# Performance work log

Hardware: AMD Instinct MI355X
Metric: run time of the kernel (lower is better)

## Reference

```python
import jax, jax.numpy as jnp
import numpy as np

B, N, M = 4, 2048, 2048
DIM, DIM_KEYS, DIM_OUT = 512, 512, 512
HEADS, DIM_HEAD = 8, 64
INNER = HEADS * DIM_HEAD


def setup_inputs() -> dict:
    key = jax.random.key(0)
    ks = jax.random.split(key, 8)
    x = jax.random.normal(ks[0], (B, N, DIM), dtype=jnp.float32)
    context = jax.random.normal(ks[1], (B, M, DIM_KEYS), dtype=jnp.float32)
    Wq = jax.random.normal(ks[2], (DIM, INNER), dtype=jnp.float32) / np.sqrt(DIM)
    Wkv = jax.random.normal(ks[3], (DIM_KEYS, 2 * INNER), dtype=jnp.float32) / np.sqrt(DIM_KEYS)
    null_k = jax.random.normal(ks[4], (DIM_HEAD,), dtype=jnp.float32)
    null_v = jax.random.normal(ks[5], (DIM_HEAD,), dtype=jnp.float32)
    Wout = jax.random.normal(ks[6], (INNER, DIM_OUT), dtype=jnp.float32) / np.sqrt(INNER)
    bout = jnp.zeros((DIM_OUT,), dtype=jnp.float32)
    return {"x": x, "context": context, "Wq": Wq, "Wkv": Wkv,
            "null_k": null_k, "null_v": null_v, "Wout": Wout, "bout": bout}


def reference(x, context, Wq, Wkv, null_k, null_v, Wout, bout):
    b = x.shape[0]
    scale = DIM_HEAD ** (-0.5)
    q = x @ Wq                      # [b, n, inner]
    kv = context @ Wkv              # [b, m, 2*inner]
    k, v = jnp.split(kv, 2, axis=-1)
    # [b, h, n, d]
    q = q.reshape(b, -1, HEADS, DIM_HEAD).transpose(0, 2, 1, 3)
    k = k.reshape(b, -1, HEADS, DIM_HEAD).transpose(0, 2, 1, 3)
    v = v.reshape(b, -1, HEADS, DIM_HEAD).transpose(0, 2, 1, 3)
    # prepend null key/value token: [b, h, 1, d]
    nk = jnp.broadcast_to(null_k, (b, HEADS, 1, DIM_HEAD))
    nv = jnp.broadcast_to(null_v, (b, HEADS, 1, DIM_HEAD))
    k = jnp.concatenate((nk, k), axis=-2)  # [b, h, m+1, d]
    v = jnp.concatenate((nv, v), axis=-2)
    q = jnp.tanh(q)
    k = jnp.tanh(k)
    sim = jnp.einsum('bhid,bhjd->bhij', q, k) * scale  # [b, h, n, m+1]
    attn = jax.nn.softmax(sim, axis=-1)
    out = jnp.einsum('bhij,bhjd->bhid', attn, v)       # [b, h, n, d]
    out = out.transpose(0, 2, 1, 3).reshape(b, -1, INNER)  # [b, n, inner]
    return out @ Wout + bout
```

## Files before the change

kernel.cpp:

```cpp
#include <hip/hip_runtime.h>
#include <hip/hip_bf16.h>
#include <stdint.h>

#define B_    4
#define N_    2048
#define M_    2048
#define DIMX  512
#define INNER 512
#define H_    8
#define DH    64
#define MK    2049
#define MKP   2112

#define QSCALE  0.18033688011f
#define SM_BIAS -11.5415605f

using u16 = unsigned short;
using u32 = unsigned int;

typedef __attribute__((ext_vector_type(8))) short short8;
typedef __attribute__((ext_vector_type(4))) float f32x4;

#if defined(__has_builtin)
# if __has_builtin(__builtin_amdgcn_exp2f)
#  define EXP2(x) __builtin_amdgcn_exp2f(x)
# endif
#endif
#ifndef EXP2
# define EXP2(x) exp2f(x)
#endif

__device__ __forceinline__ u16 bfc(float f){
  __hip_bfloat16 h = __float2bfloat16(f);
  return *reinterpret_cast<u16*>(&h);
}
__device__ __forceinline__ u32 bfpk(float lo, float hi){
  return (u32)bfc(lo) | ((u32)bfc(hi) << 16);
}
__device__ __forceinline__ u32 bfpk_tr(float lo, float hi){
  union { float f; u32 u; } a, b; a.f = lo; b.f = hi;
  return (a.u >> 16) | (b.u & 0xffff0000u);
}

__global__ __launch_bounds__(256) void prep(
    const float* __restrict__ x, const float* __restrict__ ctx,
    const float* __restrict__ Wq, const float* __restrict__ Wkv,
    const float* __restrict__ Wout,
    u16* __restrict__ xb, u16* __restrict__ cb,
    u16* __restrict__ Wqt, u16* __restrict__ Wkvt, u16* __restrict__ Woutt)
{
  const int bid = blockIdx.x;
  if (bid < 4096){
    const float* in = (bid < 2048) ? x : ctx;
    u16* out        = (bid < 2048) ? xb : cb;
    const int i = (bid & 2047) * 256 + threadIdx.x;
    float4 a = ((const float4*)in)[i*2];
    float4 b = ((const float4*)in)[i*2+1];
    uint4 t;
    t.x = bfpk(a.x, a.y); t.y = bfpk(a.z, a.w);
    t.z = bfpk(b.x, b.y); t.w = bfpk(b.z, b.w);
    ((uint4*)out)[i] = t;
    return;
  }
  const int tt = bid - 4096;
  const int z  = tt >> 7;
  const int rem = tt & 127;
  const int cx = rem & 15, ry = rem >> 4;
  const float* in = (z == 0) ? Wq : (z == 1) ? Wkv : Wout;
  u16* out        = (z == 0) ? Wqt : (z == 1) ? Wkvt : Woutt;
  const int C     = (z == 1) ? 1024 : 512;
  const int R     = 512;
  if (cx * 64 >= C) return;

  __shared__ float tl[64][65];
  const int t = threadIdx.x;
  const int c0 = cx * 64, r0 = ry * 64;
  const int col = t & 63, rb = t >> 6;
  #pragma unroll
  for (int j = 0; j < 16; ++j){
    const int row = rb + j*4;
    tl[row][col] = in[(size_t)(r0 + row) * C + c0 + col];
  }
  __syncthreads();
  #pragma unroll
  for (int j = 0; j < 16; ++j){
    const int orow = rb + j*4;
    out[(size_t)(c0 + orow) * R + r0 + col] = bfc(tl[col][orow]);
  }
}

#define PROJ_COMPUTE(bi)                                                      \
  {                                                                           \
    short8 af[4], bf[4];                                                      \
    _Pragma("unroll")                                                         \
    for (int m = 0; m < 4; ++m){                                              \
      const int row = wr + m*16 + c;                                          \
      af[m] = *(const short8*)((char*)At[bi] + row*64 + ((g ^ ((row>>1)&3)) << 4)); \
    }                                                                         \
    _Pragma("unroll")                                                         \
    for (int n = 0; n < 4; ++n){                                              \
      const int row = wc + n*16 + c;                                          \
      bf[n] = *(const short8*)((char*)Bl[bi] + row*64 + ((g ^ ((row>>1)&3)) << 4)); \
    }                                                                         \
    __builtin_amdgcn_s_setprio(1);                                            \
    _Pragma("unroll")                                                         \
    for (int m = 0; m < 4; ++m)                                               \
      _Pragma("unroll")                                                       \
      for (int n = 0; n < 4; ++n)                                             \
        acc[m][n] = __builtin_amdgcn_mfma_f32_16x16x32_bf16(af[m], bf[n], acc[m][n], 0, 0, 0); \
    __builtin_amdgcn_s_setprio(0);                                            \
  }

__global__ __launch_bounds__(256, 3) void fused_proj(
    const u16* __restrict__ xb, const u16* __restrict__ cb,
    const u16* __restrict__ Wqt, const u16* __restrict__ Wkvt,
    u16* __restrict__ qb, u16* __restrict__ kb, u16* __restrict__ vb)
{
  __shared__ __align__(16) short At[2][128*32];
  __shared__ __align__(16) short Bl[2][128*32];

  const int flat = blockIdx.x;
  const int tile = (flat & 7) * 96 + (flat >> 3);
  const bool isq = tile < 256;
  const int lt   = isq ? tile : tile - 256;
  const int gx   = isq ? 4 : 8;
  const int row0 = (lt / gx) * 128, col0 = (lt % gx) * 128;
  const u16* A  = isq ? xb : cb;
  const u16* Bt = isq ? Wqt : Wkvt;

  const int tid = threadIdx.x;
  const int w = tid >> 6, lane = tid & 63;
  const int c = lane & 15, g = lane >> 4;
  const int wr = (w >> 1) * 64, wc = (w & 1) * 64;

  f32x4 acc[4][4] = {};

  const int srow = tid >> 1, sj = (tid & 1) * 2;
  const int swz0 = ((sj  ) ^ ((srow >> 1) & 3)) << 4;
  const int swz1 = ((sj+1) ^ ((srow >> 1) & 3)) << 4;

  const u16* asrc = A  + (size_t)(row0 + srow) * DIMX + sj*8;
  const u16* bsrc = Bt + (size_t)(col0 + srow) * DIMX + sj*8;

  uint4 aA0, aA1, bA0, bA1;
  uint4 aB0, aB1, bB0, bB1;

  aA0 = ((const uint4*)asrc)[0];        aA1 = ((const uint4*)asrc)[1];
  bA0 = ((const uint4*)bsrc)[0];        bA1 = ((const uint4*)bsrc)[1];
  aB0 = ((const uint4*)(asrc + 32))[0]; aB1 = ((const uint4*)(asrc + 32))[1];
  bB0 = ((const uint4*)(bsrc + 32))[0]; bB1 = ((const uint4*)(bsrc + 32))[1];
  *(uint4*)((char*)At[0] + srow*64 + swz0) = aA0;
  *(uint4*)((char*)At[0] + srow*64 + swz1) = aA1;
  *(uint4*)((char*)Bl[0] + srow*64 + swz0) = bA0;
  *(uint4*)((char*)Bl[0] + srow*64 + swz1) = bA1;

  for (int kk = 0; kk < 16; kk += 2){
    __syncthreads();
    if (kk + 2 < 16){
      const u16* an = asrc + (kk+2)*32;
      const u16* bn = bsrc + (kk+2)*32;
      aA0 = ((const uint4*)an)[0]; aA1 = ((const uint4*)an)[1];
      bA0 = ((const uint4*)bn)[0]; bA1 = ((const uint4*)bn)[1];
    }
    PROJ_COMPUTE(0);
    *(uint4*)((char*)At[1] + srow*64 + swz0) = aB0;
    *(uint4*)((char*)At[1] + srow*64 + swz1) = aB1;
    *(uint4*)((char*)Bl[1] + srow*64 + swz0) = bB0;
    *(uint4*)((char*)Bl[1] + srow*64 + swz1) = bB1;

    __syncthreads();
    if (kk + 3 < 16){
      const u16* an = asrc + (kk+3)*32;
      const u16* bn = bsrc + (kk+3)*32;
      aB0 = ((const uint4*)an)[0]; aB1 = ((const uint4*)an)[1];
      bB0 = ((const uint4*)bn)[0]; bB1 = ((const uint4*)bn)[1];
    }
    PROJ_COMPUTE(1);
    if (kk + 2 < 16){
      *(uint4*)((char*)At[0] + srow*64 + swz0) = aA0;
      *(uint4*)((char*)At[0] + srow*64 + swz1) = aA1;
      *(uint4*)((char*)Bl[0] + srow*64 + swz0) = bA0;
      *(uint4*)((char*)Bl[0] + srow*64 + swz1) = bA1;
    }
  }

  #pragma unroll
  for (int m = 0; m < 4; ++m){
    #pragma unroll
    for (int n = 0; n < 4; ++n){
      #pragma unroll
      for (int rr = 0; rr < 4; ++rr){
        const int R = row0 + wr + m*16 + g*4 + rr;
        const int col = col0 + wc + n*16 + c;
        const float v = acc[m][n][rr];
        if (isq){
          qb[(size_t)R * INNER + col] = bfc(tanhf(v) * QSCALE);
        } else {
          const int bidx = R >> 11, mm = R & 2047;
          if (col < INNER){
            const int h = col >> 6, d = col & 63;
            kb[((size_t)(bidx*H_ + h) * MKP + (mm + 1)) * DH + d] = bfc(tanhf(v));
          } else {
            const int cc = col - INNER;
            const int h = cc >> 6, d = cc & 63;
            vb[((size_t)(bidx*H_ + h) * MKP + (mm + 1)) * DH + d] = bfc(v);
          }
        }
      }
    }
  }
}

__global__ __launch_bounds__(256, 3) void mgemm_out(
    const u16* __restrict__ A, const u16* __restrict__ Bt,
    float* __restrict__ Cf, const float* __restrict__ bias)
{
  __shared__ __align__(16) short At[2][128*32];
  __shared__ __align__(16) short Bl[2][64*32];

  const int flat = blockIdx.x;
  const int tile = (flat & 7) * 64 + (flat >> 3);
  const int row0 = (tile >> 3) * 128, col0 = (tile & 7) * 64;

  const int tid = threadIdx.x;
  const int w = tid >> 6, lane = tid & 63;
  const int c = lane & 15, g = lane >> 4;
  const int wr = (w >> 1) * 64, wc = (w & 1) * 32;

  f32x4 acc[4][2] = {};

  const int srow = tid >> 1, sj = (tid & 1) * 2;
  const int swz0 = ((sj  ) ^ ((srow >> 1) & 3)) << 4;
  const int swz1 = ((sj+1) ^ ((srow >> 1) & 3)) << 4;
  const int brow = tid >> 2, bch = tid & 3;
  const int bswz = (bch ^ ((brow >> 1) & 3)) << 4;

  const u16* asrc = A  + (size_t)(row0 + srow) * INNER + sj*8;
  const u16* bsrc = Bt + (size_t)(col0 + brow) * INNER + bch*8;

  uint4 aA0, aA1, bA0;
  uint4 aB0, aB1, bB0;

  aA0 = ((const uint4*)asrc)[0];        aA1 = ((const uint4*)asrc)[1];
  bA0 = *(const uint4*)bsrc;
  aB0 = ((const uint4*)(asrc + 32))[0]; aB1 = ((const uint4*)(asrc + 32))[1];
  bB0 = *(const uint4*)(bsrc + 32);
  *(uint4*)((char*)At[0] + srow*64 + swz0) = aA0;
  *(uint4*)((char*)At[0] + srow*64 + swz1) = aA1;
  *(uint4*)((char*)Bl[0] + brow*64 + bswz) = bA0;

  for (int kk = 0; kk < 16; kk += 2){
    __syncthreads();
    if (kk + 2 < 16){
      const u16* an = asrc + (kk+2)*32;
      aA0 = ((const uint4*)an)[0]; aA1 = ((const uint4*)an)[1];
      bA0 = *(const uint4*)(bsrc + (kk+2)*32);
    }
    {
      short8 af[4], bf[2];
      #pragma unroll
      for (int m = 0; m < 4; ++m){
        const int row = wr + m*16 + c;
        af[m] = *(const short8*)((char*)At[0] + row*64 + ((g ^ ((row>>1)&3)) << 4));
      }
      #pragma unroll
      for (int n = 0; n < 2; ++n){
        const int row = wc + n*16 + c;
        bf[n] = *(const short8*)((char*)Bl[0] + row*64 + ((g ^ ((row>>1)&3)) << 4));
      }
      __builtin_amdgcn_s_setprio(1);
      #pragma unroll
      for (int m = 0; m < 4; ++m)
        #pragma unroll
        for (int n = 0; n < 2; ++n)
          acc[m][n] = __builtin_amdgcn_mfma_f32_16x16x32_bf16(af[m], bf[n], acc[m][n], 0, 0, 0);
      __builtin_amdgcn_s_setprio(0);
    }
    *(uint4*)((char*)At[1] + srow*64 + swz0) = aB0;
    *(uint4*)((char*)At[1] + srow*64 + swz1) = aB1;
    *(uint4*)((char*)Bl[1] + brow*64 + bswz) = bB0;

    __syncthreads();
    if (kk + 3 < 16){
      const u16* an = asrc + (kk+3)*32;
      aB0 = ((const uint4*)an)[0]; aB1 = ((const uint4*)an)[1];
      bB0 = *(const uint4*)(bsrc + (kk+3)*32);
    }
    {
      short8 af[4], bf[2];
      #pragma unroll
      for (int m = 0; m < 4; ++m){
        const int row = wr + m*16 + c;
        af[m] = *(const short8*)((char*)At[1] + row*64 + ((g ^ ((row>>1)&3)) << 4));
      }
      #pragma unroll
      for (int n = 0; n < 2; ++n){
        const int row = wc + n*16 + c;
        bf[n] = *(const short8*)((char*)Bl[1] + row*64 + ((g ^ ((row>>1)&3)) << 4));
      }
      __builtin_amdgcn_s_setprio(1);
      #pragma unroll
      for (int m = 0; m < 4; ++m)
        #pragma unroll
        for (int n = 0; n < 2; ++n)
          acc[m][n] = __builtin_amdgcn_mfma_f32_16x16x32_bf16(af[m], bf[n], acc[m][n], 0, 0, 0);
      __builtin_amdgcn_s_setprio(0);
    }
    if (kk + 2 < 16){
      *(uint4*)((char*)At[0] + srow*64 + swz0) = aA0;
      *(uint4*)((char*)At[0] + srow*64 + swz1) = aA1;
      *(uint4*)((char*)Bl[0] + brow*64 + bswz) = bA0;
    }
  }

  #pragma unroll
  for (int m = 0; m < 4; ++m){
    #pragma unroll
    for (int n = 0; n < 2; ++n){
      #pragma unroll
      for (int rr = 0; rr < 4; ++rr){
        const int R = row0 + wr + m*16 + g*4 + rr;
        const int col = col0 + wc + n*16 + c;
        Cf[(size_t)R * 512 + col] = acc[m][n][rr] + bias[col];
      }
    }
  }
}

__global__ __launch_bounds__(256) void vtrans(
    const u16* __restrict__ vb, u16* __restrict__ vt,
    const float* __restrict__ nk, const float* __restrict__ nv,
    u16* __restrict__ kb)
{
  __shared__ short tl[64][72];
  const int t = threadIdx.x;
  const int mt = blockIdx.x, bh = blockIdx.y;
  {
    const int mr = t >> 2, chb = (t & 3) * 2;
    const u16* src = vb + ((size_t)bh * MKP + mt*64 + mr) * DH + chb*8;
    uint4 a = ((const uint4*)src)[0];
    uint4 b = ((const uint4*)src)[1];
    *(uint4*)((char*)tl + mr*144 + chb*16)     = a;
    *(uint4*)((char*)tl + mr*144 + (chb+1)*16) = b;
  }
  __syncthreads();
  {
    const int d = t >> 2, chb = (t & 3) * 2;
    #pragma unroll
    for (int j = 0; j < 2; ++j){
      const int mbase = (chb + j) * 8;
      u16 s[8];
      #pragma unroll
      for (int e = 0; e < 8; ++e) s[e] = (u16)tl[mbase + e][d];
      if (mt == 0 && mbase == 0) s[0] = bfc(nv[d]);
      uint4 o;
      o.x = (u32)s[0] | ((u32)s[1] << 16);
      o.y = (u32)s[2] | ((u32)s[3] << 16);
      o.z = (u32)s[4] | ((u32)s[5] << 16);
      o.w = (u32)s[6] | ((u32)s[7] << 16);
      *(uint4*)(vt + ((size_t)bh * DH + d) * MKP + mt*64 + mbase) = o;
    }
    if (mt == 0 && (t & 3) == 0)
      kb[(size_t)bh * MKP * DH + d] = bfc(tanhf(nk[d]));
  }
}

__global__ __launch_bounds__(256) void attn_mfma(
    const u16* __restrict__ qb, const u16* __restrict__ kb,
    const u16* __restrict__ vt, u16* __restrict__ aob)
{
  __shared__ __align__(16) short Kl[2][64*64];
  __shared__ __align__(16) short Vl[2][64*64];
  __shared__ __align__(16) short Pl[4][32*64];

  const int tid  = threadIdx.x;
  const int w    = tid >> 6;
  const int lane = tid & 63;
  const int c    = lane & 15;
  const int g    = lane >> 4;
  const int bh   = blockIdx.y, b = bh >> 3, h = bh & 7;
  const int qbase = blockIdx.x * 128 + w * 32;
  const int xr   = (c & 7) << 4;

  short8 qf[2][2];
  #pragma unroll
  for (int u = 0; u < 2; ++u){
    const u16* qrow = qb + ((size_t)(b*N_) + qbase + u*16 + c) * INNER + h * DH;
    qf[u][0] = *(const short8*)(qrow + g*8);
    qf[u][1] = *(const short8*)(qrow + 32 + g*8);
  }

  f32x4 o[2][4] = {};
  f32x4 lacc[2] = {};
  const short8 ones = {0x3F80,0x3F80,0x3F80,0x3F80,0x3F80,0x3F80,0x3F80,0x3F80};

  const u16* kbase = kb + (size_t)bh * MKP * DH;
  const u16* vbase = vt + (size_t)bh * DH * MKP;
  const int srow = tid >> 2, sch = (tid & 3) * 2;
  const int swz0 = ((sch  ) ^ (srow & 7)) << 4;
  const int swz1 = ((sch+1) ^ (srow & 7)) << 4;

  uint4 rk0, rk1, rv0, rv1;
  {
    const u16* ksrc = kbase + (size_t)srow * DH + sch*8;
    rk0 = ((const uint4*)ksrc)[0]; rk1 = ((const uint4*)ksrc)[1];
    const u16* vsrc = vbase + (size_t)srow * MKP + sch*8;
    rv0 = ((const uint4*)vsrc)[0]; rv1 = ((const uint4*)vsrc)[1];
  }
  *(uint4*)((char*)Kl[0] + srow*128 + swz0) = rk0;
  *(uint4*)((char*)Kl[0] + srow*128 + swz1) = rk1;
  *(uint4*)((char*)Vl[0] + srow*128 + swz0) = rv0;
  *(uint4*)((char*)Vl[0] + srow*128 + swz1) = rv1;

  int cur = 0;
  for (int kt = 0; kt < 33; ++kt){
    __syncthreads();
    if (kt < 32){
      const u16* ksrc = kbase + (size_t)((kt+1)*64 + srow) * DH + sch*8;
      rk0 = ((const uint4*)ksrc)[0]; rk1 = ((const uint4*)ksrc)[1];
      const u16* vsrc = vbase + (size_t)srow * MKP + (kt+1)*64 + sch*8;
      rv0 = ((const uint4*)vsrc)[0]; rv1 = ((const uint4*)vsrc)[1];
    }

    const char* Kc = (const char*)Kl[cur];
    const char* Vc = (const char*)Vl[cur];
    char*       Pw = (char*)Pl + w*4096;

    f32x4 sv[2][4];
    __builtin_amdgcn_s_setprio(1);
    #pragma unroll
    for (int s = 0; s < 4; ++s){
      const int row = s*16 + c;
      short8 kf0 = *(const short8*)(Kc + row*128 + ((     g*16) ^ xr));
      short8 kf1 = *(const short8*)(Kc + row*128 + ((64 + g*16) ^ xr));
      f32x4 a0 = {SM_BIAS, SM_BIAS, SM_BIAS, SM_BIAS};
      f32x4 a1 = {SM_BIAS, SM_BIAS, SM_BIAS, SM_BIAS};
      a0 = __builtin_amdgcn_mfma_f32_16x16x32_bf16(kf0, qf[0][0], a0, 0, 0, 0);
      a1 = __builtin_amdgcn_mfma_f32_16x16x32_bf16(kf0, qf[1][0], a1, 0, 0, 0);
      a0 = __builtin_amdgcn_mfma_f32_16x16x32_bf16(kf1, qf[0][1], a0, 0, 0, 0);
      a1 = __builtin_amdgcn_mfma_f32_16x16x32_bf16(kf1, qf[1][1], a1, 0, 0, 0);
      sv[0][s] = a0; sv[1][s] = a1;
    }
    __builtin_amdgcn_s_setprio(0);

    if (kt == 32){
      #pragma unroll
      for (int u = 0; u < 2; ++u)
        #pragma unroll
        for (int s = 0; s < 4; ++s)
          #pragma unroll
          for (int r = 0; r < 4; ++r)
            if (s | r) sv[u][s][r] = -1e30f;
      if (g){ sv[0][0][0] = -1e30f; sv[1][0][0] = -1e30f; }
    }

    #pragma unroll
    for (int u = 0; u < 2; ++u){
      #pragma unroll
      for (int s = 0; s < 4; ++s){
        const float p0 = EXP2(sv[u][s][0]);
        const float p1 = EXP2(sv[u][s][1]);
        const float p2 = EXP2(sv[u][s][2]);
        const float p3 = EXP2(sv[u][s][3]);
        uint2 pk;
        pk.x = bfpk_tr(p0, p1);
        pk.y = bfpk_tr(p2, p3);
        *(uint2*)(Pw + (u*16 + c)*128
                  + ((((2*s + (g>>1)) ^ (c&7)) << 4) | ((g&1)*8))) = pk;
      }
    }

    __builtin_amdgcn_s_setprio(1);
    #pragma unroll
    for (int hh = 0; hh < 2; ++hh){
      short8 pf0 = *(const short8*)(Pw + (     c)*128 + (((hh*4 + g) ^ (c&7)) << 4));
      short8 pf1 = *(const short8*)(Pw + (16 + c)*128 + (((hh*4 + g) ^ (c&7)) << 4));
      lacc[0] = __builtin_amdgcn_mfma_f32_16x16x32_bf16(pf0, ones, lacc[0], 0, 0, 0);
      lacc[1] = __builtin_amdgcn_mfma_f32_16x16x32_bf16(pf1, ones, lacc[1], 0, 0, 0);
      #pragma unroll
      for (int D = 0; D < 4; ++D){
        short8 vf = *(const short8*)(Vc + (D*16 + c)*128 + ((hh*64 + g*16) ^ xr));
        o[0][D] = __builtin_amdgcn_mfma_f32_16x16x32_bf16(pf0, vf, o[0][D], 0, 0, 0);
        o[1][D] = __builtin_amdgcn_mfma_f32_16x16x32_bf16(pf1, vf, o[1][D], 0, 0, 0);
      }
    }
    __builtin_amdgcn_s_setprio(0);

    if (kt < 32){
      char* Kn = (char*)Kl[cur ^ 1];
      char* Vn = (char*)Vl[cur ^ 1];
      *(uint4*)(Kn + srow*128 + swz0) = rk0;
      *(uint4*)(Kn + srow*128 + swz1) = rk1;
      *(uint4*)(Vn + srow*128 + swz0) = rv0;
      *(uint4*)(Vn + srow*128 + swz1) = rv1;
      cur ^= 1;
    }
  }

  #pragma unroll
  for (int u = 0; u < 2; ++u){
    #pragma unroll
    for (int r = 0; r < 4; ++r){
      const float ir = 1.f / lacc[u][r];
      const size_t nrow = (size_t)(b*N_) + qbase + u*16 + g*4 + r;
      #pragma unroll
      for (int D = 0; D < 4; ++D)
        aob[nrow * INNER + h*DH + D*16 + c] = bfc(o[u][D][r] * ir);
    }
  }
}

extern "C" void kernel_launch(void* const* d_in, const int* in_sizes, int n_in,
                              void* d_out, int out_size, void* d_ws, size_t ws_size,
                              hipStream_t stream)
{
  const float* x    = (const float*)d_in[0];
  const float* ctx  = (const float*)d_in[1];
  const float* Wq   = (const float*)d_in[2];
  const float* Wkv  = (const float*)d_in[3];
  const float* nk   = (const float*)d_in[4];
  const float* nv   = (const float*)d_in[5];
  const float* Wout = (const float*)d_in[6];
  const float* bout = (const float*)d_in[7];
  float* out = (float*)d_out;

  char* ws = (char*)d_ws;
  u16* xb    = (u16*)(ws);
  u16* cb    = (u16*)(ws +  8388608);
  u16* qb    = (u16*)(ws + 16777216);
  u16* kbB   = (u16*)(ws + 25165824);
  u16* vbB   = (u16*)(ws + 33816576);
  u16* vtb   = (u16*)(ws + 42467328);
  u16* Wqt   = (u16*)(ws + 51118080);
  u16* Wkvt  = (u16*)(ws + 51642368);
  u16* Woutt = (u16*)(ws + 52690944);
  u16* aoB   = vbB;

  prep<<<4480, 256, 0, stream>>>(x, ctx, Wq, Wkv, Wout, xb, cb, Wqt, Wkvt, Woutt);

  fused_proj<<<768, 256, 0, stream>>>(xb, cb, Wqt, Wkvt, qb, kbB, vbB);
  vtrans<<<dim3(33, 32), 256, 0, stream>>>(vbB, vtb, nk, nv, kbB);
  attn_mfma<<<dim3(16, 32), 256, 0, stream>>>(qb, kbB, vtb, aoB);
  mgemm_out<<<512, 256, 0, stream>>>(aoB, Woutt, out, bout);
}
```

Baseline: 108.9 us.

## Write V transposed directly from projection epilogue and drop vtrans kernel

The projection epilogue now stores V straight into the transposed [bh, d, m] layout using packed 4-element bf16 writes. This removes the separate vtrans kernel, its extra global round trip of V and one launch. The null key/value token moves from the first to the last key slot and is written by extra blocks in the prep kernel. The attention-output buffer now reuses the dead xb region. The trade-off is that the transposed V stores from the GEMM epilogue are strided and less coalesced than the shared-memory transpose was.

```diff
diff --git a/kernel.cpp b/kernel.cpp
--- a/kernel.cpp
+++ b/kernel.cpp
@@ -46,8 +46,10 @@
     const float* __restrict__ x, const float* __restrict__ ctx,
     const float* __restrict__ Wq, const float* __restrict__ Wkv,
     const float* __restrict__ Wout,
+    const float* __restrict__ nk, const float* __restrict__ nv,
     u16* __restrict__ xb, u16* __restrict__ cb,
-    u16* __restrict__ Wqt, u16* __restrict__ Wkvt, u16* __restrict__ Woutt)
+    u16* __restrict__ Wqt, u16* __restrict__ Wkvt, u16* __restrict__ Woutt,
+    u16* __restrict__ kb, u16* __restrict__ vt)
 {
   const int bid = blockIdx.x;
   if (bid < 4096){
@@ -60,6 +62,13 @@
     t.x = bfpk(a.x, a.y); t.y = bfpk(a.z, a.w);
     t.z = bfpk(b.x, b.y); t.w = bfpk(b.z, b.w);
     ((uint4*)out)[i] = t;
+    return;
+  }
+  if (bid >= 4480){
+    const int i = (bid - 4480) * 256 + threadIdx.x;
+    const int d = i & 63, bh = i >> 6;
+    kb[((size_t)bh * MKP + 2048) * DH + d] = bfc(tanhf(nk[d]));
+    vt[((size_t)bh * DH + d) * MKP + 2048] = bfc(nv[d]);
     return;
   }
   const int tt = bid - 4096;
@@ -114,7 +123,7 @@
 __global__ __launch_bounds__(256, 3) void fused_proj(
     const u16* __restrict__ xb, const u16* __restrict__ cb,
     const u16* __restrict__ Wqt, const u16* __restrict__ Wkvt,
-    u16* __restrict__ qb, u16* __restrict__ kb, u16* __restrict__ vb)
+    u16* __restrict__ qb, u16* __restrict__ kb, u16* __restrict__ vt)
 {
   __shared__ __align__(16) short At[2][128*32];
   __shared__ __align__(16) short Bl[2][128*32];
@@ -188,23 +197,27 @@
   for (int m = 0; m < 4; ++m){
     #pragma unroll
     for (int n = 0; n < 4; ++n){
-      #pragma unroll
-      for (int rr = 0; rr < 4; ++rr){
-        const int R = row0 + wr + m*16 + g*4 + rr;
-        const int col = col0 + wc + n*16 + c;
-        const float v = acc[m][n][rr];
-        if (isq){
-          qb[(size_t)R * INNER + col] = bfc(tanhf(v) * QSCALE);
+      const int R0  = row0 + wr + m*16 + g*4;
+      const int col = col0 + wc + n*16 + c;
+      if (isq){
+        #pragma unroll
+        for (int rr = 0; rr < 4; ++rr)
+          qb[(size_t)(R0 + rr) * INNER + col] = bfc(tanhf(acc[m][n][rr]) * QSCALE);
+      } else {
+        const int bidx = R0 >> 11, mm = R0 & 2047;
+        if (col < INNER){
+          const int h = col >> 6, d = col & 63;
+          #pragma unroll
+          for (int rr = 0; rr < 4; ++rr)
+            kb[((size_t)(bidx*H_ + h) * MKP + mm + rr) * DH + d] =
+                bfc(tanhf(acc[m][n][rr]));
         } else {
-          const int bidx = R >> 11, mm = R & 2047;
-          if (col < INNER){
-            const int h = col >> 6, d = col & 63;
-            kb[((size_t)(bidx*H_ + h) * MKP + (mm + 1)) * DH + d] = bfc(tanhf(v));
-          } else {
-            const int cc = col - INNER;
-            const int h = cc >> 6, d = cc & 63;
-            vb[((size_t)(bidx*H_ + h) * MKP + (mm + 1)) * DH + d] = bfc(v);
-          }
+          const int cc = col - INNER;
+          const int h = cc >> 6, d = cc & 63;
+          uint2 o;
+          o.x = bfpk(acc[m][n][0], acc[m][n][1]);
+          o.y = bfpk(acc[m][n][2], acc[m][n][3]);
+          *(uint2*)(vt + ((size_t)(bidx*H_ + h) * DH + d) * MKP + mm) = o;
         }
       }
     }
@@ -324,44 +337,6 @@
         Cf[(size_t)R * 512 + col] = acc[m][n][rr] + bias[col];
       }
     }
-  }
-}
-
-__global__ __launch_bounds__(256) void vtrans(
-    const u16* __restrict__ vb, u16* __restrict__ vt,
-    const float* __restrict__ nk, const float* __restrict__ nv,
-    u16* __restrict__ kb)
-{
-  __shared__ short tl[64][72];
-  const int t = threadIdx.x;
-  const int mt = blockIdx.x, bh = blockIdx.y;
-  {
-    const int mr = t >> 2, chb = (t & 3) * 2;
-    const u16* src = vb + ((size_t)bh * MKP + mt*64 + mr) * DH + chb*8;
-    uint4 a = ((const uint4*)src)[0];
-    uint4 b = ((const uint4*)src)[1];
-    *(uint4*)((char*)tl + mr*144 + chb*16)     = a;
-    *(uint4*)((char*)tl + mr*144 + (chb+1)*16) = b;
-  }
-  __syncthreads();
-  {
-    const int d = t >> 2, chb = (t & 3) * 2;
-    #pragma unroll
-    for (int j = 0; j < 2; ++j){
-      const int mbase = (chb + j) * 8;
-      u16 s[8];
-      #pragma unroll
-      for (int e = 0; e < 8; ++e) s[e] = (u16)tl[mbase + e][d];
-      if (mt == 0 && mbase == 0) s[0] = bfc(nv[d]);
-      uint4 o;
-      o.x = (u32)s[0] | ((u32)s[1] << 16);
-      o.y = (u32)s[2] | ((u32)s[3] << 16);
-      o.z = (u32)s[4] | ((u32)s[5] << 16);
-      o.w = (u32)s[6] | ((u32)s[7] << 16);
-      *(uint4*)(vt + ((size_t)bh * DH + d) * MKP + mt*64 + mbase) = o;
-    }
-    if (mt == 0 && (t & 3) == 0)
-      kb[(size_t)bh * MKP * DH + d] = bfc(tanhf(nk[d]));
   }
 }
 
@@ -529,17 +504,16 @@
   u16* cb    = (u16*)(ws +  8388608);
   u16* qb    = (u16*)(ws + 16777216);
   u16* kbB   = (u16*)(ws + 25165824);
-  u16* vbB   = (u16*)(ws + 33816576);
-  u16* vtb   = (u16*)(ws + 42467328);
-  u16* Wqt   = (u16*)(ws + 51118080);
-  u16* Wkvt  = (u16*)(ws + 51642368);
-  u16* Woutt = (u16*)(ws + 52690944);
-  u16* aoB   = vbB;
-
-  prep<<<4480, 256, 0, stream>>>(x, ctx, Wq, Wkv, Wout, xb, cb, Wqt, Wkvt, Woutt);
-
-  fused_proj<<<768, 256, 0, stream>>>(xb, cb, Wqt, Wkvt, qb, kbB, vbB);
-  vtrans<<<dim3(33, 32), 256, 0, stream>>>(vbB, vtb, nk, nv, kbB);
+  u16* vtb   = (u16*)(ws + 33816576);
+  u16* Wqt   = (u16*)(ws + 42467328);
+  u16* Wkvt  = (u16*)(ws + 42991616);
+  u16* Woutt = (u16*)(ws + 44040192);
+  u16* aoB   = xb;
+
+  prep<<<4488, 256, 0, stream>>>(x, ctx, Wq, Wkv, Wout, nk, nv,
+                                 xb, cb, Wqt, Wkvt, Woutt, kbB, vtb);
+
+  fused_proj<<<768, 256, 0, stream>>>(xb, cb, Wqt, Wkvt, qb, kbB, vtb);
   attn_mfma<<<dim3(16, 32), 256, 0, stream>>>(qb, kbB, vtb, aoB);
   mgemm_out<<<512, 256, 0, stream>>>(aoB, Woutt, out, bout);
 }
```

Result: faster. 101.1 us, median of 2 (-7.1%).
